# Performance work log

Hardware: AMD Instinct MI355X
Metric: run time of the kernel (lower is better)

The kernel has to match this reference:

```python
import jax, jax.numpy as jnp
import numpy as np

IN_C = 256
OUT_C = 256
HID = IN_C * 2
N_POINTS = 262144
N_NODES = 8192
B = 16
MAX_NODES = 512
EPS = 1e-5


def _mlp(h, w1, b1, g1, be1, w2, b2):
    # PyG MLP([C, 2C, out], norm='layer_norm'): lin -> layernorm -> relu -> (dropout, eval=identity) -> lin
    h = h @ w1 + b1
    mu = jnp.mean(h, axis=-1, keepdims=True)
    var = jnp.var(h, axis=-1, keepdims=True)
    h = (h - mu) * jax.lax.rsqrt(var + EPS) * g1 + be1
    h = jax.nn.relu(h)
    return h @ w2 + b2


def setup_inputs() -> dict:
    key = jax.random.key(0)
    ks = jax.random.split(key, 16)
    x = jax.random.normal(ks[0], (N_POINTS, IN_C), dtype=jnp.float32)
    f_point_batches = jnp.sort(jax.random.randint(ks[1], (N_POINTS,), 0, N_NODES)).astype(jnp.int32)
    # equal-sized graphs (16 graphs x 512 nodes), sorted as torch.split/pad_sequence assume
    g_node_batches = jnp.repeat(jnp.arange(B, dtype=jnp.int32), MAX_NODES)
    s = 1.0 / np.sqrt(IN_C)
    s2 = 1.0 / np.sqrt(HID)
    def lin(k, fan_in, shape, scale):
        return jax.random.uniform(k, shape, jnp.float32, -scale, scale)
    params = {}
    for i, name in enumerate(['Wq', 'Wk']):
        base = 2 + i * 6
        params[f'{name}_w1'] = lin(ks[base + 0], IN_C, (IN_C, HID), s)
        params[f'{name}_b1'] = lin(ks[base + 1], IN_C, (HID,), s)
        params[f'{name}_g1'] = jnp.ones((HID,), jnp.float32)
        params[f'{name}_be1'] = jnp.zeros((HID,), jnp.float32)
        params[f'{name}_w2'] = lin(ks[base + 2], HID, (HID, OUT_C), s2)
        params[f'{name}_b2'] = lin(ks[base + 3], HID, (OUT_C,), s2)
    return dict(x=x, f_point_batches=f_point_batches, g_node_batches=g_node_batches,
                num_graphs=B, max_nodes=MAX_NODES, **params)


def reference(x, f_point_batches, g_node_batches, num_graphs, max_nodes,
              Wq_w1, Wq_b1, Wq_g1, Wq_be1, Wq_w2, Wq_b2,
              Wk_w1, Wk_b1, Wk_g1, Wk_be1, Wk_w2, Wk_b2):
    n_nodes = g_node_batches.shape[0]
    C = x.shape[1]
    # scatter_mean over points -> per-node feature means [n_nodes, C]
    sums = jax.ops.segment_sum(x, f_point_batches, num_segments=n_nodes)
    cnt = jax.ops.segment_sum(jnp.ones((x.shape[0],), x.dtype), f_point_batches, num_segments=n_nodes)
    mean = sums / jnp.maximum(cnt, 1.0)[:, None]
    # ragged split by graph + pad_sequence -> [B, max_nodes, C]
    starts = jnp.searchsorted(g_node_batches, jnp.arange(num_graphs, dtype=g_node_batches.dtype))
    pos = jnp.arange(n_nodes) - starts[g_node_batches]
    padded = jnp.zeros((num_graphs, max_nodes, C), x.dtype).at[g_node_batches, pos].set(mean, mode='drop')
    q = _mlp(padded, Wq_w1, Wq_b1, Wq_g1, Wq_be1, Wq_w2, Wq_b2)  # [B, MAXN, out]
    k = _mlp(padded, Wk_w1, Wk_b1, Wk_g1, Wk_be1, Wk_w2, Wk_b2)
    return jnp.einsum('bnd,bmd->bnm', q, k)  # bmm(q, k^T)
```

## Files before the change

kernel.cpp:

```cpp
#include <hip/hip_runtime.h>
#include <hip/hip_bf16.h>

#define N_POINTS 262144
#define N_NODES  8192
#define IN_C     256
#define HID      512
#define OUT_C    256
#define NB       16
#define MAXN     512
#define EPSV     1e-5f

typedef __attribute__((ext_vector_type(8))) short short8;
typedef __attribute__((ext_vector_type(4))) float f32x4;
#define MFMA16(a, b, c) __builtin_amdgcn_mfma_f32_16x16x32_bf16((a), (b), (c), 0, 0, 0)


__global__ __launch_bounds__(256) void prelude_k(
    const int* __restrict__ fpb, int* __restrict__ starts,
    const float* __restrict__ W1q, const float* __restrict__ W1k,
    const float* __restrict__ W2q, const float* __restrict__ W2k,
    __hip_bfloat16* __restrict__ P1q, __hip_bfloat16* __restrict__ P1k,
    __hip_bfloat16* __restrict__ P2q, __hip_bfloat16* __restrict__ P2k)
{
  if (blockIdx.x < 1024) {
    const int i = blockIdx.x * 256 + threadIdx.x;
    const int cur = fpb[i];
    const int prev = (i == 0) ? -1 : fpb[i - 1];
    for (int n = prev + 1; n <= cur; ++n) starts[n] = i;
    if (i == N_POINTS - 1)
      for (int n = cur + 1; n <= N_NODES; ++n) starts[n] = N_POINTS;
    return;
  }
  const int bid = blockIdx.x - 1024;
  const int sel = bid >> 6;
  const float* W; __hip_bfloat16* P; int N;
  switch (sel) {
    case 0:  W = W1q; P = P1q; N = HID;   break;
    case 1:  W = W1k; P = P1k; N = HID;   break;
    case 2:  W = W2q; P = P2q; N = OUT_C; break;
    default: W = W2k; P = P2k; N = OUT_C; break;
  }
  const int idx = (bid & 63) * 256 + threadIdx.x;
  const int NF = N >> 4;
  const int lane = idx & 63;
  const int nf = (idx >> 6) % NF;
  const int ks = idx / (64 * NF);
  const int k0 = ks * 32 + (lane >> 4) * 8;
  const int n  = nf * 16 + (lane & 15);
  __hip_bfloat16 tmp[8];
  #pragma unroll
  for (int j = 0; j < 8; ++j) tmp[j] = __float2bfloat16(W[(size_t)(k0 + j) * N + n]);
  *(uint4*)(P + (size_t)idx * 8) = *(uint4*)tmp;
}

__global__ __launch_bounds__(256) void scatter_mean_k(
    const float* __restrict__ x, const int* __restrict__ starts,
    __hip_bfloat16* __restrict__ mean)
{
  const int node = blockIdx.x;
  const int start = starts[node];
  const int end   = starts[node + 1];
  const int t  = threadIdx.x;
  const int c4 = t & 63;
  const int rr = t >> 6;

  float4 s = make_float4(0.f, 0.f, 0.f, 0.f);
  for (int r = start + rr; r < end; r += 4) {
    float4 v = *(const float4*)(x + (size_t)r * IN_C + c4 * 4);
    s.x += v.x; s.y += v.y; s.z += v.z; s.w += v.w;
  }

  __shared__ float4 red[256];
  red[t] = s;
  __syncthreads();
  if (t < 64) {
    float4 a = red[t], b = red[t + 64], c = red[t + 128], d = red[t + 192];
    const int cnt = end - start;
    const float inv = cnt > 0 ? 1.0f / (float)cnt : 0.0f;
    __hip_bfloat16 o[4];
    o[0] = __float2bfloat16((a.x + b.x + c.x + d.x) * inv);
    o[1] = __float2bfloat16((a.y + b.y + c.y + d.y) * inv);
    o[2] = __float2bfloat16((a.z + b.z + c.z + d.z) * inv);
    o[3] = __float2bfloat16((a.w + b.w + c.w + d.w) * inv);
    *(uint2*)(mean + (size_t)node * IN_C + t * 4) = *(uint2*)o;
  }
}

__global__ __launch_bounds__(256, 2) void mlp_fused_k(
    const __hip_bfloat16* __restrict__ mean,
    const __hip_bfloat16* __restrict__ P1q, const __hip_bfloat16* __restrict__ P2q,
    const float* __restrict__ b1q, const float* __restrict__ g1q,
    const float* __restrict__ be1q, const float* __restrict__ b2q,
    const __hip_bfloat16* __restrict__ P1k, const __hip_bfloat16* __restrict__ P2k,
    const float* __restrict__ b1k, const float* __restrict__ g1k,
    const float* __restrict__ be1k, const float* __restrict__ b2k,
    __hip_bfloat16* __restrict__ qo, __hip_bfloat16* __restrict__ ko)
{
  const int head = blockIdx.y;
  const __hip_bfloat16* P1 = head ? P1k : P1q;
  const __hip_bfloat16* P2 = head ? P2k : P2q;
  const float* b1  = head ? b1k  : b1q;
  const float* g1  = head ? g1k  : g1q;
  const float* be1 = head ? be1k : be1q;
  const float* b2  = head ? b2k  : b2q;
  __hip_bfloat16* out = head ? ko : qo;

  const int row0 = blockIdx.x * 64;
  const int t = threadIdx.x;
  const int w  = t >> 6;
  const int l  = t & 63;
  const int lg = l >> 4;
  const int lm = l & 15;

  __shared__ __hip_bfloat16 HsRaw[64 * 520];
  __shared__ float lnp[4][64][2];
  __hip_bfloat16* As = HsRaw;

  #pragma unroll
  for (int it = 0; it < 8; ++it) {
    const int idx = t + it * 256;
    const int r = idx >> 5, c8 = idx & 31;
    uint4 v = *(const uint4*)(mean + (size_t)(row0 + r) * IN_C + c8 * 8);
    *(uint4*)(As + r * 264 + c8 * 8) = v;
  }
  __syncthreads();

  f32x4 acc1[4][8];
  #pragma unroll
  for (int mi = 0; mi < 4; ++mi)
    #pragma unroll
    for (int nj = 0; nj < 8; ++nj)
      #pragma unroll
      for (int r = 0; r < 4; ++r) acc1[mi][nj][r] = 0.f;

  for (int ks = 0; ks < 8; ++ks) {
    short8 a[4], b[8];
    #pragma unroll
    for (int mi = 0; mi < 4; ++mi)
      a[mi] = *(const short8*)(As + (mi * 16 + lm) * 264 + ks * 32 + lg * 8);
    const __hip_bfloat16* bp = P1 + ((size_t)(ks * 32 + w * 8) * 64 + l) * 8;
    #pragma unroll
    for (int nj = 0; nj < 8; ++nj)
      b[nj] = *(const short8*)(bp + (size_t)nj * 64 * 8);
    #pragma unroll
    for (int mi = 0; mi < 4; ++mi)
      #pragma unroll
      for (int nj = 0; nj < 8; ++nj)
        acc1[mi][nj] = MFMA16(a[mi], b[nj], acc1[mi][nj]);
  }

  float b1v[8], g1v[8], e1v[8];
  #pragma unroll
  for (int nj = 0; nj < 8; ++nj) {
    const int c = w * 128 + nj * 16 + lm;
    b1v[nj] = b1[c]; g1v[nj] = g1[c]; e1v[nj] = be1[c];
  }
  #pragma unroll
  for (int mi = 0; mi < 4; ++mi)
    #pragma unroll
    for (int nj = 0; nj < 8; ++nj)
      #pragma unroll
      for (int r = 0; r < 4; ++r) acc1[mi][nj][r] += b1v[nj];

  float sums[4][4], sqs[4][4];
  #pragma unroll
  for (int mi = 0; mi < 4; ++mi)
    #pragma unroll
    for (int r = 0; r < 4; ++r) {
      float s = 0.f, q = 0.f;
      #pragma unroll
      for (int nj = 0; nj < 8; ++nj) {
        const float xv = acc1[mi][nj][r];
        s += xv; q += xv * xv;
      }
      #pragma unroll
      for (int off = 1; off < 16; off <<= 1) {
        s += __shfl_xor(s, off);
        q += __shfl_xor(q, off);
      }
      sums[mi][r] = s; sqs[mi][r] = q;
    }
  if (lm == 0) {
    #pragma unroll
    for (int mi = 0; mi < 4; ++mi)
      #pragma unroll
      for (int r = 0; r < 4; ++r) {
        const int row = mi * 16 + lg * 4 + r;
        lnp[w][row][0] = sums[mi][r];
        lnp[w][row][1] = sqs[mi][r];
      }
  }
  __syncthreads();

  #pragma unroll
  for (int mi = 0; mi < 4; ++mi) {
    #pragma unroll
    for (int r = 0; r < 4; ++r) {
      const int row = mi * 16 + lg * 4 + r;
      float S = 0.f, Q = 0.f;
      #pragma unroll
      for (int w2 = 0; w2 < 4; ++w2) { S += lnp[w2][row][0]; Q += lnp[w2][row][1]; }
      const float mu = S * (1.0f / HID);
      const float var = Q * (1.0f / HID) - mu * mu;
      const float rs = rsqrtf(var + EPSV);
      #pragma unroll
      for (int nj = 0; nj < 8; ++nj) {
        const float y = (acc1[mi][nj][r] - mu) * rs * g1v[nj] + e1v[nj];
        HsRaw[row * 520 + w * 128 + nj * 16 + lm] = __float2bfloat16(fmaxf(y, 0.f));
      }
    }
  }
  __syncthreads();

  f32x4 acc2[4][4];
  #pragma unroll
  for (int mi = 0; mi < 4; ++mi)
    #pragma unroll
    for (int nj = 0; nj < 4; ++nj)
      #pragma unroll
      for (int r = 0; r < 4; ++r) acc2[mi][nj][r] = 0.f;

  for (int ks = 0; ks < 16; ++ks) {
    short8 a2[4], b2f[4];
    #pragma unroll
    for (int mi = 0; mi < 4; ++mi)
      a2[mi] = *(const short8*)(HsRaw + (mi * 16 + lm) * 520 + ks * 32 + lg * 8);
    const __hip_bfloat16* bp2 = P2 + ((size_t)(ks * 16 + w * 4) * 64 + l) * 8;
    #pragma unroll
    for (int nj = 0; nj < 4; ++nj)
      b2f[nj] = *(const short8*)(bp2 + (size_t)nj * 64 * 8);
    #pragma unroll
    for (int mi = 0; mi < 4; ++mi)
      #pragma unroll
      for (int nj = 0; nj < 4; ++nj)
        acc2[mi][nj] = MFMA16(a2[mi], b2f[nj], acc2[mi][nj]);
  }

  float b2v[4];
  #pragma unroll
  for (int nj = 0; nj < 4; ++nj) b2v[nj] = b2[w * 64 + nj * 16 + lm];
  #pragma unroll
  for (int mi = 0; mi < 4; ++mi)
    #pragma unroll
    for (int nj = 0; nj < 4; ++nj)
      #pragma unroll
      for (int r = 0; r < 4; ++r) {
        const int row = row0 + mi * 16 + lg * 4 + r;
        const int col = w * 64 + nj * 16 + lm;
        out[(size_t)row * OUT_C + col] = __float2bfloat16(acc2[mi][nj][r] + b2v[nj]);
      }
}

__global__ __launch_bounds__(256) void bmm_k(
    const __hip_bfloat16* __restrict__ q, const __hip_bfloat16* __restrict__ k,
    float* __restrict__ out)
{
  const int b  = blockIdx.z;
  const int n0 = blockIdx.x * 128;
  const int m0 = blockIdx.y * 128;
  const int t = threadIdx.x;
  const int w = t >> 6, l = t & 63, lg = l >> 4, lm = l & 15;
  const int wm = w >> 1, wn = w & 1;

  const __hip_bfloat16* qb = q + ((size_t)b * MAXN + n0 + wm * 64) * OUT_C;
  const __hip_bfloat16* kb = k + ((size_t)b * MAXN + m0 + wn * 64) * OUT_C;

  f32x4 acc[4][4];
  #pragma unroll
  for (int mi = 0; mi < 4; ++mi)
    #pragma unroll
    for (int nj = 0; nj < 4; ++nj)
      #pragma unroll
      for (int r = 0; r < 4; ++r) acc[mi][nj][r] = 0.f;

  for (int ks = 0; ks < 8; ++ks) {
    short8 a[4], bb[4];
    #pragma unroll
    for (int mi = 0; mi < 4; ++mi)
      a[mi] = *(const short8*)(qb + (size_t)(mi * 16 + lm) * OUT_C + ks * 32 + lg * 8);
    #pragma unroll
    for (int nj = 0; nj < 4; ++nj)
      bb[nj] = *(const short8*)(kb + (size_t)(nj * 16 + lm) * OUT_C + ks * 32 + lg * 8);
    #pragma unroll
    for (int mi = 0; mi < 4; ++mi)
      #pragma unroll
      for (int nj = 0; nj < 4; ++nj)
        acc[mi][nj] = MFMA16(a[mi], bb[nj], acc[mi][nj]);
  }

  #pragma unroll
  for (int mi = 0; mi < 4; ++mi)
    #pragma unroll
    for (int nj = 0; nj < 4; ++nj)
      #pragma unroll
      for (int r = 0; r < 4; ++r) {
        const int nrow = n0 + wm * 64 + mi * 16 + lg * 4 + r;
        const int mcol = m0 + wn * 64 + nj * 16 + lm;
        out[((size_t)b * MAXN + nrow) * MAXN + mcol] = acc[mi][nj][r];
      }
}

extern "C" void kernel_launch(void* const* d_in, const int* in_sizes, int n_in,
                              void* d_out, int out_size, void* d_ws, size_t ws_size,
                              hipStream_t stream)
{
  const float* x   = (const float*)d_in[0];
  const int*   fpb = (const int*)d_in[1];
  const float* Wq_w1  = (const float*)d_in[5];
  const float* Wq_b1  = (const float*)d_in[6];
  const float* Wq_g1  = (const float*)d_in[7];
  const float* Wq_be1 = (const float*)d_in[8];
  const float* Wq_w2  = (const float*)d_in[9];
  const float* Wq_b2  = (const float*)d_in[10];
  const float* Wk_w1  = (const float*)d_in[11];
  const float* Wk_b1  = (const float*)d_in[12];
  const float* Wk_g1  = (const float*)d_in[13];
  const float* Wk_be1 = (const float*)d_in[14];
  const float* Wk_w2  = (const float*)d_in[15];
  const float* Wk_b2  = (const float*)d_in[16];

  __hip_bfloat16* ws = (__hip_bfloat16*)d_ws;
  __hip_bfloat16* P1q  = ws;
  __hip_bfloat16* P1k  = P1q + 131072;
  __hip_bfloat16* P2q  = P1k + 131072;
  __hip_bfloat16* P2k  = P2q + 131072;
  __hip_bfloat16* mean = P2k + 131072;
  __hip_bfloat16* qo   = mean + 2097152;
  __hip_bfloat16* ko   = qo + 2097152;
  int* starts = (int*)(ko + 2097152);
  float* out = (float*)d_out;

  prelude_k<<<1280, 256, 0, stream>>>(fpb, starts,
      Wq_w1, Wk_w1, Wq_w2, Wk_w2, P1q, P1k, P2q, P2k);
  scatter_mean_k<<<N_NODES, 256, 0, stream>>>(x, starts, mean);
  mlp_fused_k<<<dim3(N_NODES / 64, 2), 256, 0, stream>>>(
      mean, P1q, P2q, Wq_b1, Wq_g1, Wq_be1, Wq_b2,
      P1k, P2k, Wk_b1, Wk_g1, Wk_be1, Wk_b2, qo, ko);
  bmm_k<<<dim3(4, 4, NB), 256, 0, stream>>>(qo, ko, out);
}
```

Baseline: 102.0 us.

## Fuse scatter-mean into MLP kernel and compute both q/k heads per block

Merges the per-node scatter-mean into the MLP kernel, so each block reduces the points of 16 nodes straight into shared memory and the bf16 mean buffer round-trip and one launch go away. Each block now processes both the q and k heads for its 16 rows, sharing the A operand. The cost is that the row tile shrinks from 64 to 16, so every block re-reads the full packed weights for only 16 rows, which greatly raises weight traffic (mostly L2). Each wave also reduces its points serially per node, giving less parallelism than the old 256-thread-per-node scatter.

```diff
diff --git a/kernel.cpp b/kernel.cpp
--- a/kernel.cpp
+++ b/kernel.cpp
@@ -9,6 +9,7 @@
 #define NB       16
 #define MAXN     512
 #define EPSV     1e-5f
+#define NPB      16
 
 typedef __attribute__((ext_vector_type(8))) short short8;
 typedef __attribute__((ext_vector_type(4))) float f32x4;
@@ -53,41 +54,8 @@
   *(uint4*)(P + (size_t)idx * 8) = *(uint4*)tmp;
 }
 
-__global__ __launch_bounds__(256) void scatter_mean_k(
+__global__ __launch_bounds__(256, 2) void fused_mlp_k(
     const float* __restrict__ x, const int* __restrict__ starts,
-    __hip_bfloat16* __restrict__ mean)
-{
-  const int node = blockIdx.x;
-  const int start = starts[node];
-  const int end   = starts[node + 1];
-  const int t  = threadIdx.x;
-  const int c4 = t & 63;
-  const int rr = t >> 6;
-
-  float4 s = make_float4(0.f, 0.f, 0.f, 0.f);
-  for (int r = start + rr; r < end; r += 4) {
-    float4 v = *(const float4*)(x + (size_t)r * IN_C + c4 * 4);
-    s.x += v.x; s.y += v.y; s.z += v.z; s.w += v.w;
-  }
-
-  __shared__ float4 red[256];
-  red[t] = s;
-  __syncthreads();
-  if (t < 64) {
-    float4 a = red[t], b = red[t + 64], c = red[t + 128], d = red[t + 192];
-    const int cnt = end - start;
-    const float inv = cnt > 0 ? 1.0f / (float)cnt : 0.0f;
-    __hip_bfloat16 o[4];
-    o[0] = __float2bfloat16((a.x + b.x + c.x + d.x) * inv);
-    o[1] = __float2bfloat16((a.y + b.y + c.y + d.y) * inv);
-    o[2] = __float2bfloat16((a.z + b.z + c.z + d.z) * inv);
-    o[3] = __float2bfloat16((a.w + b.w + c.w + d.w) * inv);
-    *(uint2*)(mean + (size_t)node * IN_C + t * 4) = *(uint2*)o;
-  }
-}
-
-__global__ __launch_bounds__(256, 2) void mlp_fused_k(
-    const __hip_bfloat16* __restrict__ mean,
     const __hip_bfloat16* __restrict__ P1q, const __hip_bfloat16* __restrict__ P2q,
     const float* __restrict__ b1q, const float* __restrict__ g1q,
     const float* __restrict__ be1q, const float* __restrict__ b2q,
@@ -96,159 +64,148 @@
     const float* __restrict__ be1k, const float* __restrict__ b2k,
     __hip_bfloat16* __restrict__ qo, __hip_bfloat16* __restrict__ ko)
 {
-  const int head = blockIdx.y;
-  const __hip_bfloat16* P1 = head ? P1k : P1q;
-  const __hip_bfloat16* P2 = head ? P2k : P2q;
-  const float* b1  = head ? b1k  : b1q;
-  const float* g1  = head ? g1k  : g1q;
-  const float* be1 = head ? be1k : be1q;
-  const float* b2  = head ? b2k  : b2q;
-  __hip_bfloat16* out = head ? ko : qo;
-
-  const int row0 = blockIdx.x * 64;
+  const int n0 = blockIdx.x * NPB;
   const int t = threadIdx.x;
-  const int w  = t >> 6;
-  const int l  = t & 63;
-  const int lg = l >> 4;
-  const int lm = l & 15;
-
-  __shared__ __hip_bfloat16 HsRaw[64 * 520];
-  __shared__ float lnp[4][64][2];
-  __hip_bfloat16* As = HsRaw;
-
-  #pragma unroll
-  for (int it = 0; it < 8; ++it) {
-    const int idx = t + it * 256;
-    const int r = idx >> 5, c8 = idx & 31;
-    uint4 v = *(const uint4*)(mean + (size_t)(row0 + r) * IN_C + c8 * 8);
-    *(uint4*)(As + r * 264 + c8 * 8) = v;
+  const int w = t >> 6, l = t & 63, lg = l >> 4, lm = l & 15;
+
+  __shared__ __hip_bfloat16 As[NPB * 264];
+  __shared__ __hip_bfloat16 Hq[NPB * 520];
+  __shared__ __hip_bfloat16 Hk[NPB * 520];
+  __shared__ float lnpq[4][NPB][2];
+  __shared__ float lnpk[4][NPB][2];
+
+  #pragma unroll
+  for (int i = 0; i < 4; ++i) {
+    const int nl = w * 4 + i;
+    const int node = n0 + nl;
+    const int s_ = starts[node], e_ = starts[node + 1];
+    float4 s = make_float4(0.f, 0.f, 0.f, 0.f);
+    for (int r = s_; r < e_; ++r) {
+      float4 v = *(const float4*)(x + (size_t)r * IN_C + l * 4);
+      s.x += v.x; s.y += v.y; s.z += v.z; s.w += v.w;
+    }
+    const int cnt = e_ - s_;
+    const float inv = cnt > 0 ? 1.0f / (float)cnt : 0.0f;
+    __hip_bfloat16 o[4];
+    o[0] = __float2bfloat16(s.x * inv);
+    o[1] = __float2bfloat16(s.y * inv);
+    o[2] = __float2bfloat16(s.z * inv);
+    o[3] = __float2bfloat16(s.w * inv);
+    *(uint2*)(As + nl * 264 + l * 4) = *(uint2*)o;
   }
   __syncthreads();
 
-  f32x4 acc1[4][8];
-  #pragma unroll
-  for (int mi = 0; mi < 4; ++mi)
-    #pragma unroll
-    for (int nj = 0; nj < 8; ++nj)
-      #pragma unroll
-      for (int r = 0; r < 4; ++r) acc1[mi][nj][r] = 0.f;
+  f32x4 aq[8], ak[8];
+  #pragma unroll
+  for (int nj = 0; nj < 8; ++nj)
+    #pragma unroll
+    for (int r = 0; r < 4; ++r) { aq[nj][r] = 0.f; ak[nj][r] = 0.f; }
 
   for (int ks = 0; ks < 8; ++ks) {
-    short8 a[4], b[8];
-    #pragma unroll
-    for (int mi = 0; mi < 4; ++mi)
-      a[mi] = *(const short8*)(As + (mi * 16 + lm) * 264 + ks * 32 + lg * 8);
-    const __hip_bfloat16* bp = P1 + ((size_t)(ks * 32 + w * 8) * 64 + l) * 8;
-    #pragma unroll
-    for (int nj = 0; nj < 8; ++nj)
-      b[nj] = *(const short8*)(bp + (size_t)nj * 64 * 8);
-    #pragma unroll
-    for (int mi = 0; mi < 4; ++mi)
-      #pragma unroll
-      for (int nj = 0; nj < 8; ++nj)
-        acc1[mi][nj] = MFMA16(a[mi], b[nj], acc1[mi][nj]);
-  }
-
-  float b1v[8], g1v[8], e1v[8];
+    short8 a = *(const short8*)(As + lm * 264 + ks * 32 + lg * 8);
+    const __hip_bfloat16* bpq = P1q + ((size_t)(ks * 32 + w * 8) * 64 + l) * 8;
+    const __hip_bfloat16* bpk = P1k + ((size_t)(ks * 32 + w * 8) * 64 + l) * 8;
+    #pragma unroll
+    for (int nj = 0; nj < 8; ++nj) {
+      short8 bq = *(const short8*)(bpq + (size_t)nj * 512);
+      short8 bk = *(const short8*)(bpk + (size_t)nj * 512);
+      aq[nj] = MFMA16(a, bq, aq[nj]);
+      ak[nj] = MFMA16(a, bk, ak[nj]);
+    }
+  }
+
+  float b1vq[8], g1vq[8], e1vq[8], b1vk[8], g1vk[8], e1vk[8];
   #pragma unroll
   for (int nj = 0; nj < 8; ++nj) {
     const int c = w * 128 + nj * 16 + lm;
-    b1v[nj] = b1[c]; g1v[nj] = g1[c]; e1v[nj] = be1[c];
-  }
-  #pragma unroll
-  for (int mi = 0; mi < 4; ++mi)
-    #pragma unroll
-    for (int nj = 0; nj < 8; ++nj)
-      #pragma unroll
-      for (int r = 0; r < 4; ++r) acc1[mi][nj][r] += b1v[nj];
-
-  float sums[4][4], sqs[4][4];
-  #pragma unroll
-  for (int mi = 0; mi < 4; ++mi)
+    b1vq[nj] = b1q[c]; g1vq[nj] = g1q[c]; e1vq[nj] = be1q[c];
+    b1vk[nj] = b1k[c]; g1vk[nj] = g1k[c]; e1vk[nj] = be1k[c];
+  }
+  #pragma unroll
+  for (int nj = 0; nj < 8; ++nj)
+    #pragma unroll
+    for (int r = 0; r < 4; ++r) { aq[nj][r] += b1vq[nj]; ak[nj][r] += b1vk[nj]; }
+
+  #pragma unroll
+  for (int r = 0; r < 4; ++r) {
+    float sq = 0.f, qq = 0.f, sk = 0.f, qk = 0.f;
+    #pragma unroll
+    for (int nj = 0; nj < 8; ++nj) {
+      const float vq = aq[nj][r], vk = ak[nj][r];
+      sq += vq; qq += vq * vq;
+      sk += vk; qk += vk * vk;
+    }
+    #pragma unroll
+    for (int off = 1; off < 16; off <<= 1) {
+      sq += __shfl_xor(sq, off); qq += __shfl_xor(qq, off);
+      sk += __shfl_xor(sk, off); qk += __shfl_xor(qk, off);
+    }
+    if (lm == 0) {
+      const int row = lg * 4 + r;
+      lnpq[w][row][0] = sq; lnpq[w][row][1] = qq;
+      lnpk[w][row][0] = sk; lnpk[w][row][1] = qk;
+    }
+  }
+  __syncthreads();
+
+  #pragma unroll
+  for (int r = 0; r < 4; ++r) {
+    const int row = lg * 4 + r;
+    float Sq = 0.f, Qq = 0.f, Sk = 0.f, Qk = 0.f;
+    #pragma unroll
+    for (int w2 = 0; w2 < 4; ++w2) {
+      Sq += lnpq[w2][row][0]; Qq += lnpq[w2][row][1];
+      Sk += lnpk[w2][row][0]; Qk += lnpk[w2][row][1];
+    }
+    const float muq = Sq * (1.0f / HID);
+    const float rsq = rsqrtf(Qq * (1.0f / HID) - muq * muq + EPSV);
+    const float muk = Sk * (1.0f / HID);
+    const float rsk = rsqrtf(Qk * (1.0f / HID) - muk * muk + EPSV);
+    #pragma unroll
+    for (int nj = 0; nj < 8; ++nj) {
+      const float yq = (aq[nj][r] - muq) * rsq * g1vq[nj] + e1vq[nj];
+      const float yk = (ak[nj][r] - muk) * rsk * g1vk[nj] + e1vk[nj];
+      Hq[row * 520 + w * 128 + nj * 16 + lm] = __float2bfloat16(fmaxf(yq, 0.f));
+      Hk[row * 520 + w * 128 + nj * 16 + lm] = __float2bfloat16(fmaxf(yk, 0.f));
+    }
+  }
+  __syncthreads();
+
+  f32x4 cq[4], ck[4];
+  #pragma unroll
+  for (int nj = 0; nj < 4; ++nj)
+    #pragma unroll
+    for (int r = 0; r < 4; ++r) { cq[nj][r] = 0.f; ck[nj][r] = 0.f; }
+
+  for (int ks = 0; ks < 16; ++ks) {
+    short8 a2q = *(const short8*)(Hq + lm * 520 + ks * 32 + lg * 8);
+    short8 a2k = *(const short8*)(Hk + lm * 520 + ks * 32 + lg * 8);
+    const __hip_bfloat16* bpq2 = P2q + ((size_t)(ks * 16 + w * 4) * 64 + l) * 8;
+    const __hip_bfloat16* bpk2 = P2k + ((size_t)(ks * 16 + w * 4) * 64 + l) * 8;
+    #pragma unroll
+    for (int nj = 0; nj < 4; ++nj) {
+      short8 bq = *(const short8*)(bpq2 + (size_t)nj * 512);
+      short8 bk = *(const short8*)(bpk2 + (size_t)nj * 512);
+      cq[nj] = MFMA16(a2q, bq, cq[nj]);
+      ck[nj] = MFMA16(a2k, bk, ck[nj]);
+    }
+  }
+
+  float b2vq[4], b2vk[4];
+  #pragma unroll
+  for (int nj = 0; nj < 4; ++nj) {
+    b2vq[nj] = b2q[w * 64 + nj * 16 + lm];
+    b2vk[nj] = b2k[w * 64 + nj * 16 + lm];
+  }
+  #pragma unroll
+  for (int nj = 0; nj < 4; ++nj)
     #pragma unroll
     for (int r = 0; r < 4; ++r) {
-      float s = 0.f, q = 0.f;
-      #pragma unroll
-      for (int nj = 0; nj < 8; ++nj) {
-        const float xv = acc1[mi][nj][r];
-        s += xv; q += xv * xv;
-      }
-      #pragma unroll
-      for (int off = 1; off < 16; off <<= 1) {
-        s += __shfl_xor(s, off);
-        q += __shfl_xor(q, off);
-      }
-      sums[mi][r] = s; sqs[mi][r] = q;
-    }
-  if (lm == 0) {
-    #pragma unroll
-    for (int mi = 0; mi < 4; ++mi)
-      #pragma unroll
-      for (int r = 0; r < 4; ++r) {
-        const int row = mi * 16 + lg * 4 + r;
-        lnp[w][row][0] = sums[mi][r];
-        lnp[w][row][1] = sqs[mi][r];
-      }
-  }
-  __syncthreads();
-
-  #pragma unroll
-  for (int mi = 0; mi < 4; ++mi) {
-    #pragma unroll
-    for (int r = 0; r < 4; ++r) {
-      const int row = mi * 16 + lg * 4 + r;
-      float S = 0.f, Q = 0.f;
-      #pragma unroll
-      for (int w2 = 0; w2 < 4; ++w2) { S += lnp[w2][row][0]; Q += lnp[w2][row][1]; }
-      const float mu = S * (1.0f / HID);
-      const float var = Q * (1.0f / HID) - mu * mu;
-      const float rs = rsqrtf(var + EPSV);
-      #pragma unroll
-      for (int nj = 0; nj < 8; ++nj) {
-        const float y = (acc1[mi][nj][r] - mu) * rs * g1v[nj] + e1v[nj];
-        HsRaw[row * 520 + w * 128 + nj * 16 + lm] = __float2bfloat16(fmaxf(y, 0.f));
-      }
-    }
-  }
-  __syncthreads();
-
-  f32x4 acc2[4][4];
-  #pragma unroll
-  for (int mi = 0; mi < 4; ++mi)
-    #pragma unroll
-    for (int nj = 0; nj < 4; ++nj)
-      #pragma unroll
-      for (int r = 0; r < 4; ++r) acc2[mi][nj][r] = 0.f;
-
-  for (int ks = 0; ks < 16; ++ks) {
-    short8 a2[4], b2f[4];
-    #pragma unroll
-    for (int mi = 0; mi < 4; ++mi)
-      a2[mi] = *(const short8*)(HsRaw + (mi * 16 + lm) * 520 + ks * 32 + lg * 8);
-    const __hip_bfloat16* bp2 = P2 + ((size_t)(ks * 16 + w * 4) * 64 + l) * 8;
-    #pragma unroll
-    for (int nj = 0; nj < 4; ++nj)
-      b2f[nj] = *(const short8*)(bp2 + (size_t)nj * 64 * 8);
-    #pragma unroll
-    for (int mi = 0; mi < 4; ++mi)
-      #pragma unroll
-      for (int nj = 0; nj < 4; ++nj)
-        acc2[mi][nj] = MFMA16(a2[mi], b2f[nj], acc2[mi][nj]);
-  }
-
-  float b2v[4];
-  #pragma unroll
-  for (int nj = 0; nj < 4; ++nj) b2v[nj] = b2[w * 64 + nj * 16 + lm];
-  #pragma unroll
-  for (int mi = 0; mi < 4; ++mi)
-    #pragma unroll
-    for (int nj = 0; nj < 4; ++nj)
-      #pragma unroll
-      for (int r = 0; r < 4; ++r) {
-        const int row = row0 + mi * 16 + lg * 4 + r;
-        const int col = w * 64 + nj * 16 + lm;
-        out[(size_t)row * OUT_C + col] = __float2bfloat16(acc2[mi][nj][r] + b2v[nj]);
-      }
+      const int row = n0 + lg * 4 + r;
+      const int col = w * 64 + nj * 16 + lm;
+      qo[(size_t)row * OUT_C + col] = __float2bfloat16(cq[nj][r] + b2vq[nj]);
+      ko[(size_t)row * OUT_C + col] = __float2bfloat16(ck[nj][r] + b2vk[nj]);
+    }
 }
 
 __global__ __launch_bounds__(256) void bmm_k(
@@ -324,17 +281,15 @@
   __hip_bfloat16* P1k  = P1q + 131072;
   __hip_bfloat16* P2q  = P1k + 131072;
   __hip_bfloat16* P2k  = P2q + 131072;
-  __hip_bfloat16* mean = P2k + 131072;
-  __hip_bfloat16* qo   = mean + 2097152;
+  __hip_bfloat16* qo   = P2k + 131072;
   __hip_bfloat16* ko   = qo + 2097152;
   int* starts = (int*)(ko + 2097152);
   float* out = (float*)d_out;
 
   prelude_k<<<1280, 256, 0, stream>>>(fpb, starts,
       Wq_w1, Wk_w1, Wq_w2, Wk_w2, P1q, P1k, P2q, P2k);
-  scatter_mean_k<<<N_NODES, 256, 0, stream>>>(x, starts, mean);
-  mlp_fused_k<<<dim3(N_NODES / 64, 2), 256, 0, stream>>>(
-      mean, P1q, P2q, Wq_b1, Wq_g1, Wq_be1, Wq_b2,
+  fused_mlp_k<<<N_NODES / NPB, 256, 0, stream>>>(
+      x, starts, P1q, P2q, Wq_b1, Wq_g1, Wq_be1, Wq_b2,
       P1k, P2k, Wk_b1, Wk_g1, Wk_be1, Wk_b2, qo, ko);
   bmm_k<<<dim3(4, 4, NB), 256, 0, stream>>>(qo, ko, out);
 }
```

Measured after the change: 121.9 us. 19.5% more time.
